# Kernel tuning notes

Measured on AMD Instinct MI355X. Metric: run time of the kernel, lower is better.

Reference implementation:

```python
import jax, jax.numpy as jnp
import numpy as np

N_NODES = 100000
N_EDGES = 1600000
HIDDEN = 128
HALF = HIDDEN // 2
LN_EPS = 1e-5


def setup_inputs() -> dict:
    key = jax.random.key(0)
    ks = jax.random.split(key, 8)
    pos = jax.random.normal(ks[0], (N_NODES, 3), dtype=jnp.float32) * 10.0
    edge_index = jax.random.randint(ks[1], (2, N_EDGES), 0, N_NODES, dtype=jnp.int64)
    batch = jnp.zeros((N_NODES,), dtype=jnp.int64)
    # spatial_encoder params: Linear(3, HALF) -> LayerNorm(HALF) -> GELU -> Linear(HALF, HALF)
    W1 = jax.random.normal(ks[2], (3, HALF), dtype=jnp.float32) * 0.3
    b1 = jax.random.normal(ks[3], (HALF,), dtype=jnp.float32) * 0.05
    ln_g = jnp.ones((HALF,), dtype=jnp.float32)
    ln_b = jnp.zeros((HALF,), dtype=jnp.float32)
    W2 = jax.random.normal(ks[4], (HALF, HALF), dtype=jnp.float32) * 0.1
    b2 = jax.random.normal(ks[5], (HALF,), dtype=jnp.float32) * 0.05
    return {"pos": pos, "edge_index": edge_index, "batch": batch,
            "W1": W1, "b1": b1, "ln_g": ln_g, "ln_b": ln_b, "W2": W2, "b2": b2}


def _layernorm(x, g, b):
    mu = jnp.mean(x, axis=-1, keepdims=True)
    var = jnp.mean((x - mu) ** 2, axis=-1, keepdims=True)
    return (x - mu) * jax.lax.rsqrt(var + LN_EPS) * g + b


def reference(pos, edge_index, batch, W1, b1, ln_g, ln_b, W2, b2):
    num_nodes = pos.shape[0]
    src, dst = edge_index[0], edge_index[1]
    rel = pos[dst] - pos[src]                              # [E, 3]
    dist = jnp.linalg.norm(rel, axis=1, keepdims=True)     # [E, 1]
    rel_n = rel / (dist + 1e-6)
    h = rel_n @ W1 + b1                                    # [E, HALF]
    h = _layernorm(h, ln_g, ln_b)
    h = jax.nn.gelu(h, approximate=False)                  # torch exact GELU
    code = h @ W2 + b2                                     # dropout is identity in eval
    agg = jax.ops.segment_sum(code, dst, num_segments=num_nodes)          # [N, HALF]
    deg = jax.ops.segment_sum(jnp.ones_like(dst, dtype=code.dtype), dst,
                              num_segments=num_nodes)
    deg = jnp.clip(deg, 1.0)
    agg = agg / deg[:, None]
    # original buffer is [N, HIDDEN]; only the first HALF channels receive updates
    out = jnp.concatenate([agg, jnp.zeros_like(agg)], axis=1)             # [N, HIDDEN]
    return out
```

## Files before the change

### kernel.cpp

```cpp
#include <hip/hip_runtime.h>
#include <math.h>

#define HALF 64
#define LN_EPS 1e-5f
#define TCAP 1024
#define PCAP 128

#define GC0 -2.3022082f
#define GC1 -0.1029438f

typedef float f32x2 __attribute__((ext_vector_type(2)));

__device__ __forceinline__ f32x2 pk_fma(f32x2 a, f32x2 b, f32x2 c) {
    f32x2 d;
    asm("v_pk_fma_f32 %0, %1, %2, %3" : "=v"(d) : "v"(a), "v"(b), "v"(c));
    return d;
}
__device__ __forceinline__ f32x2 pk_mul(f32x2 a, f32x2 b) {
    f32x2 d;
    asm("v_pk_mul_f32 %0, %1, %2" : "=v"(d) : "v"(a), "v"(b));
    return d;
}

__device__ __forceinline__ float gelu_fast(float x) {
    const float x2 = x * x;
    const float z  = x * fmaf(GC1, x2, GC0);
    const float e  = __builtin_amdgcn_exp2f(z);
    const float sg = __builtin_amdgcn_rcpf(1.0f + e);
    return x * sg;
}

__global__ void __launch_bounds__(256, 8) bin_kernel(
    const int* __restrict__ ei, int* __restrict__ tcount,
    unsigned* __restrict__ tbuf,
    const float* __restrict__ W1, const float* __restrict__ b1,
    float* __restrict__ fp, int E, int ntile)
{
    if (blockIdx.x == 0 && threadIdx.x < 64) {
        const int t = threadIdx.x;
        const float w0 = W1[t], w1 = W1[HALF + t], w2 = W1[2 * HALF + t], bb = b1[t];
        float v[14] = { w0, w1, w2, bb,
                        w0 * w0, w0 * w1, w0 * w2, w1 * w1, w1 * w2, w2 * w2,
                        w0 * bb, w1 * bb, w2 * bb, bb * bb };
#pragma unroll
        for (int j = 0; j < 14; ++j) {
            float s = v[j];
#pragma unroll
            for (int off = 32; off; off >>= 1) s += __shfl_down(s, off, 64);
            if (t == 0) fp[j] = s * (1.0f / 64.0f);
        }
    }

    const int p = blockIdx.x & 7;
    const int e4 = (blockIdx.x * 256 + threadIdx.x) * 4;
    if (e4 >= E) return;
    if (e4 + 3 < E) {
        const int4 s = *(const int4*)(ei + e4);
        const int4 d = *(const int4*)(ei + E + e4);
        const int t0 = d.x >> 4, t1 = d.y >> 4, t2 = d.z >> 4, t3 = d.w >> 4;
        const int s0 = atomicAdd(&tcount[(size_t)p * ntile + t0], 1);
        const int s1 = atomicAdd(&tcount[(size_t)p * ntile + t1], 1);
        const int s2 = atomicAdd(&tcount[(size_t)p * ntile + t2], 1);
        const int s3 = atomicAdd(&tcount[(size_t)p * ntile + t3], 1);
        if (s0 < PCAP)
            tbuf[((size_t)p * ntile + t0) * PCAP + s0] = ((unsigned)s.x << 4) | (d.x & 15);
        if (s1 < PCAP)
            tbuf[((size_t)p * ntile + t1) * PCAP + s1] = ((unsigned)s.y << 4) | (d.y & 15);
        if (s2 < PCAP)
            tbuf[((size_t)p * ntile + t2) * PCAP + s2] = ((unsigned)s.z << 4) | (d.z & 15);
        if (s3 < PCAP)
            tbuf[((size_t)p * ntile + t3) * PCAP + s3] = ((unsigned)s.w << 4) | (d.w & 15);
    } else {
        for (int e = e4; e < E; ++e) {
            const int d = ei[E + e];
            const int t = d >> 4;
            const int sl = atomicAdd(&tcount[(size_t)p * ntile + t], 1);
            if (sl < PCAP)
                tbuf[((size_t)p * ntile + t) * PCAP + sl] =
                    ((unsigned)ei[e] << 4) | (d & 15);
        }
    }
}

__global__ void __launch_bounds__(256, 6) nodeout_kernel(
    const unsigned* __restrict__ tbuf,
    const int* __restrict__ tcount,
    const float* __restrict__ pos,
    const float* __restrict__ W1, const float* __restrict__ b1,
    const float* __restrict__ ln_g, const float* __restrict__ ln_b,
    const float* __restrict__ W2, const float* __restrict__ b2,
    const float* __restrict__ fp,
    float* __restrict__ out, int N, int ntile)
{
    __shared__ __attribute__((aligned(16))) float sRx[TCAP + 64];
    __shared__ __attribute__((aligned(16))) float sRy[TCAP + 64];
    __shared__ __attribute__((aligned(16))) float sRz[TCAP + 64];
    __shared__ __attribute__((aligned(16))) float sRw[TCAP + 64];
    __shared__ __attribute__((aligned(16))) float sh[16 * 64];
    __shared__ float4 sPd[16];
    __shared__ int   lcnt[16], lofs[16], lcur[16];
    __shared__ int   pOff[9];

    const int tid = threadIdx.x;
    const int lane = tid & 63, w = tid >> 6;
    const int tile = blockIdx.x;
    const int base = tile * 16;

    if (tid < 16) {
        lcnt[tid] = 0;
        const int n = base + tid;
        if (n < N)
            sPd[tid] = make_float4(pos[3 * n], pos[3 * n + 1], pos[3 * n + 2], 0.0f);
    }
    if (tid < 8) {
        int c = tcount[(size_t)tid * ntile + tile];
        c = (c < PCAP) ? c : PCAP;
        int inc = c;
#pragma unroll
        for (int off = 1; off < 8; off <<= 1) {
            const int u = __shfl_up(inc, off, 64);
            if (tid >= off) inc += u;
        }
        pOff[tid + 1] = inc;
        if (tid == 0) pOff[0] = 0;
    }

    const float gl = ln_g[lane];
    const float C0 = gl * (W1[lane]            - fp[0]);
    const float C1 = gl * (W1[HALF + lane]     - fp[1]);
    const float C2 = gl * (W1[2 * HALF + lane] - fp[2]);
    const float C3 = gl * (b1[lane]            - fp[3]);
    const float Bl = ln_b[lane];
    const float b2l = b2[lane];
    const f32x2 C0p = { C0, C0 }, C1p = { C1, C1 };
    const f32x2 C2p = { C2, C2 }, C3p = { C3, C3 };
    const f32x2 Blp = { Bl, Bl };
    const f32x2 GC0p = { GC0, GC0 }, GC1p = { GC1, GC1 };

    const float ux = fp[0], uy = fp[1], uz = fp[2], cc = fp[3];
    const float Gxx = fp[4], Gxy = fp[5], Gxz = fp[6];
    const float Gyy = fp[7], Gyz = fp[8], Gzz = fp[9];
    const float px = fp[10], py = fp[11], pz = fp[12], q13 = fp[13];

    __syncthreads();
    const int cnt = pOff[8];

    unsigned ev0 = 0, ev1 = 0, ev2 = 0, ev3 = 0;
#define LOADE(EV, J)                                                        \
    if ((J) < cnt) {                                                        \
        int p = 0;                                                          \
        _Pragma("unroll")                                                   \
        for (int k = 1; k < 8; ++k) p += ((J) >= pOff[k]) ? 1 : 0;          \
        EV = tbuf[((size_t)p * ntile + tile) * PCAP + ((J) - pOff[p])];     \
        atomicAdd(&lcnt[EV & 15], 1);                                       \
    }
    LOADE(ev0, tid)
    LOADE(ev1, tid + 256)
    LOADE(ev2, tid + 512)
    LOADE(ev3, tid + 768)
#undef LOADE
    __syncthreads();

    if (tid < 16) {
        const int v = lcnt[tid];
        const int vp = (v + 3) & ~3;
        int inc = vp;
#pragma unroll
        for (int off = 1; off < 16; off <<= 1) {
            const int u = __shfl_up(inc, off, 64);
            if (tid >= off) inc += u;
        }
        lofs[tid] = inc - vp;
        lcur[tid] = inc - vp;
    }
    __syncthreads();

#define GEOM(EV, J)                                                         \
    if ((J) < cnt) {                                                        \
        const int s  = (int)((EV) >> 4);                                    \
        const int dl = (int)((EV) & 15);                                    \
        const float4 pd = sPd[dl];                                          \
        const float rx0 = pd.x - pos[3 * s];                                \
        const float ry0 = pd.y - pos[3 * s + 1];                            \
        const float rz0 = pd.z - pos[3 * s + 2];                            \
        const float dist = sqrtf(rx0 * rx0 + ry0 * ry0 + rz0 * rz0);        \
        const float invd = 1.0f / (dist + 1e-6f);                           \
        const float rx = rx0 * invd, ry = ry0 * invd, rz = rz0 * invd;      \
        const float mu  = fmaf(ux, rx, fmaf(uy, ry, fmaf(uz, rz, cc)));     \
        const float ev2 = Gxx * rx * rx + Gyy * ry * ry + Gzz * rz * rz     \
                        + 2.0f * (Gxy * rx * ry + Gxz * rx * rz             \
                                  + Gyz * ry * rz + px * rx + py * ry       \
                                  + pz * rz) + q13;                         \
        const float rstd = rsqrtf(ev2 - mu * mu + LN_EPS);                  \
        const int slot = atomicAdd(&lcur[dl], 1);                           \
        sRx[slot] = rx * rstd;                                              \
        sRy[slot] = ry * rstd;                                              \
        sRz[slot] = rz * rstd;                                              \
        sRw[slot] = rstd;                                                   \
    }
    GEOM(ev0, tid)
    GEOM(ev1, tid + 256)
    GEOM(ev2, tid + 512)
    GEOM(ev3, tid + 768)
#undef GEOM
    __syncthreads();

    const int n0 = base + w * 4;
    const int c0 = lcnt[w * 4 + 0], b0 = lofs[w * 4 + 0];
    const int c1 = lcnt[w * 4 + 1], b1o = lofs[w * 4 + 1];
    const int c2 = lcnt[w * 4 + 2], b2o = lofs[w * 4 + 2];
    const int c3 = lcnt[w * 4 + 3], b3o = lofs[w * 4 + 3];

#define PAIR_GELU(RXP, RYP, RZP, RWP, GA, GB)                               \
        {                                                                   \
            const f32x2 X = pk_fma(C0p, RXP, pk_fma(C1p, RYP,               \
                              pk_fma(C2p, RZP, pk_fma(C3p, RWP, Blp))));    \
            const f32x2 x2 = pk_mul(X, X);                                  \
            const f32x2 zt = pk_fma(GC1p, x2, GC0p);                        \
            const f32x2 z  = pk_mul(X, zt);                                 \
            const float e0 = __builtin_amdgcn_exp2f(z.x);                   \
            const float e1 = __builtin_amdgcn_exp2f(z.y);                   \
            const float r0 = __builtin_amdgcn_rcpf(1.0f + e0);              \
            const float r1 = __builtin_amdgcn_rcpf(1.0f + e1);              \
            GA += X.x * r0;                                                 \
            GB += X.y * r1;                                                 \
        }

#define NODE_ACC(BO, CQ, ROW)                                               \
    {                                                                       \
        const int cntn = (CQ);                                              \
        const int bo = (BO);                                                \
        float accA = 0.0f, accB = 0.0f;                                     \
        int i = 0;                                                          \
        for (; i + 4 <= cntn; i += 4) {     \
            const float4 vx = *(const float4*)(sRx + bo + i);               \
            const float4 vy = *(const float4*)(sRy + bo + i);               \
            const float4 vz = *(const float4*)(sRz + bo + i);               \
            const float4 vw = *(const float4*)(sRw + bo + i);               \
            f32x2 rxa = { vx.x, vx.y }, rxb = { vx.z, vx.w };               \
            f32x2 rya = { vy.x, vy.y }, ryb = { vy.z, vy.w };               \
            f32x2 rza = { vz.x, vz.y }, rzb = { vz.z, vz.w };               \
            f32x2 rwa = { vw.x, vw.y }, rwb = { vw.z, vw.w };               \
            PAIR_GELU(rxa, rya, rza, rwa, accA, accB)                       \
            PAIR_GELU(rxb, ryb, rzb, rwb, accA, accB)                       \
        }                                                                   \
        for (; i < cntn; ++i) {              \
            const float x = fmaf(C0, sRx[bo + i], fmaf(C1, sRy[bo + i],     \
                              fmaf(C2, sRz[bo + i],                         \
                                   fmaf(C3, sRw[bo + i], Bl))));            \
            accA += gelu_fast(x);                                           \
        }                                                                   \
        sh[(ROW) * 64 + lane] = (cntn > 0)                                  \
            ? (accA + accB) * (1.0f / (float)cntn) : 0.0f;                  \
    }

    NODE_ACC(b0,  c0, w * 4 + 0)
    NODE_ACC(b1o, c1, w * 4 + 1)
    NODE_ACC(b2o, c2, w * 4 + 2)
    NODE_ACC(b3o, c3, w * 4 + 3)
#undef NODE_ACC
#undef PAIR_GELU

    __builtin_amdgcn_sched_barrier(0);

    f32x2 wpk[32];
#pragma unroll
    for (int k = 0; k < 32; ++k) {
        wpk[k].x = W2[(2 * k)     * HALF + lane];
        wpk[k].y = W2[(2 * k + 1) * HALF + lane];
    }

#define PHASE2(Q, CQ)                                                       \
    if (n0 + (Q) < N) {                                                     \
        const float* row = sh + (w * 4 + (Q)) * 64;                         \
        f32x2 acc = { 0.0f, 0.0f };                                         \
        _Pragma("unroll")                                                   \
        for (int k4 = 0; k4 < 16; ++k4) {                                   \
            const float4 hv = *(const float4*)(row + 4 * k4);               \
            f32x2 ha = { hv.x, hv.y }, hb = { hv.z, hv.w };                 \
            acc = pk_fma(ha, wpk[2 * k4],     acc);                         \
            acc = pk_fma(hb, wpk[2 * k4 + 1], acc);                         \
        }                                                                   \
        const float res = ((CQ) > 0) ? (acc.x + acc.y) + b2l : 0.0f;        \
        float* orow = out + (size_t)(n0 + (Q)) * (2 * HALF);                \
        orow[lane] = res;                                                   \
        orow[HALF + lane] = 0.0f;                                           \
    }

    PHASE2(0, c0)
    PHASE2(1, c1)
    PHASE2(2, c2)
    PHASE2(3, c3)
#undef PHASE2
}

extern "C" void kernel_launch(void* const* d_in, const int* in_sizes, int n_in,
                              void* d_out, int out_size, void* d_ws, size_t ws_size,
                              hipStream_t stream) {
    const float* pos = (const float*)d_in[0];
    const int*   ei  = (const int*)d_in[1];
    const float* W1  = (const float*)d_in[3];
    const float* b1  = (const float*)d_in[4];
    const float* g   = (const float*)d_in[5];
    const float* b   = (const float*)d_in[6];
    const float* W2  = (const float*)d_in[7];
    const float* b2  = (const float*)d_in[8];
    float* out = (float*)d_out;

    const int N = in_sizes[0] / 3;
    const int E = in_sizes[1] / 2;
    const int ntile = (N + 15) / 16;

    unsigned* tbuf = (unsigned*)d_ws;
    int* tcount    = (int*)(tbuf + (size_t)8 * ntile * PCAP);
    float* fparams = (float*)(tcount + (size_t)8 * ntile);

    const int eb4 = (E / 4 + 255) / 256;

    hipMemsetAsync(tcount, 0, (size_t)8 * ntile * sizeof(int), stream);
    bin_kernel<<<eb4, 256, 0, stream>>>(ei, tcount, tbuf, W1, b1, fparams,
                                        E, ntile);
    nodeout_kernel<<<ntile, 256, 0, stream>>>(tbuf, tcount, pos, W1, b1, g, b,
                                              W2, b2, fparams, out, N, ntile);
}
```

Baseline: 224.6 us.

## Balance per-wave edge work and accumulate GELU outputs via LDS atomics

Replaces the per-node bucketed layout (count, prefix scan, scatter into SoA arrays, one wave per four nodes) with an unsorted AoS float4 array that tags each edge with its local destination in the low bits of rstd. Edges are split evenly across the four waves, and per-lane GELU results are accumulated into shared node rows with LDS float atomics. The mean division moves after the W2 matvec. This removes two barriers and the wave load imbalance caused by uneven node degrees, but adds many LDS atomic adds and perturbs rstd's low mantissa bits. The launch-bounds occupancy hint also drops from 6 to 4.

```diff
diff --git a/kernel.cpp b/kernel.cpp
--- a/kernel.cpp
+++ b/kernel.cpp
@@ -82,7 +82,7 @@
     }
 }
 
-__global__ void __launch_bounds__(256, 6) nodeout_kernel(
+__global__ void __launch_bounds__(256, 4) nodeout_kernel(
     const unsigned* __restrict__ tbuf,
     const int* __restrict__ tcount,
     const float* __restrict__ pos,
@@ -92,13 +92,10 @@
     const float* __restrict__ fp,
     float* __restrict__ out, int N, int ntile)
 {
-    __shared__ __attribute__((aligned(16))) float sRx[TCAP + 64];
-    __shared__ __attribute__((aligned(16))) float sRy[TCAP + 64];
-    __shared__ __attribute__((aligned(16))) float sRz[TCAP + 64];
-    __shared__ __attribute__((aligned(16))) float sRw[TCAP + 64];
-    __shared__ __attribute__((aligned(16))) float sh[16 * 64];
+    __shared__ __attribute__((aligned(16))) float4 sA[TCAP];
+    __shared__ __attribute__((aligned(16))) float  sh[16 * 64];
     __shared__ float4 sPd[16];
-    __shared__ int   lcnt[16], lofs[16], lcur[16];
+    __shared__ int   lcnt[16];
     __shared__ int   pOff[9];
 
     const int tid = threadIdx.x;
@@ -124,6 +121,7 @@
         pOff[tid + 1] = inc;
         if (tid == 0) pOff[0] = 0;
     }
+    for (int i = tid; i < 16 * 64; i += 256) sh[i] = 0.0f;
 
     const float gl = ln_g[lane];
     const float C0 = gl * (W1[lane]            - fp[0]);
@@ -145,40 +143,14 @@
     __syncthreads();
     const int cnt = pOff[8];
 
-    unsigned ev0 = 0, ev1 = 0, ev2 = 0, ev3 = 0;
-#define LOADE(EV, J)                                                        \
+#define PREP(J)                                                             \
     if ((J) < cnt) {                                                        \
         int p = 0;                                                          \
         _Pragma("unroll")                                                   \
         for (int k = 1; k < 8; ++k) p += ((J) >= pOff[k]) ? 1 : 0;          \
-        EV = tbuf[((size_t)p * ntile + tile) * PCAP + ((J) - pOff[p])];     \
-        atomicAdd(&lcnt[EV & 15], 1);                                       \
-    }
-    LOADE(ev0, tid)
-    LOADE(ev1, tid + 256)
-    LOADE(ev2, tid + 512)
-    LOADE(ev3, tid + 768)
-#undef LOADE
-    __syncthreads();
-
-    if (tid < 16) {
-        const int v = lcnt[tid];
-        const int vp = (v + 3) & ~3;
-        int inc = vp;
-#pragma unroll
-        for (int off = 1; off < 16; off <<= 1) {
-            const int u = __shfl_up(inc, off, 64);
-            if (tid >= off) inc += u;
-        }
-        lofs[tid] = inc - vp;
-        lcur[tid] = inc - vp;
-    }
-    __syncthreads();
-
-#define GEOM(EV, J)                                                         \
-    if ((J) < cnt) {                                                        \
-        const int s  = (int)((EV) >> 4);                                    \
-        const int dl = (int)((EV) & 15);                                    \
+        const unsigned v = tbuf[((size_t)p * ntile + tile) * PCAP + ((J) - pOff[p])]; \
+        const int s  = (int)(v >> 4);                                       \
+        const int dl = (int)(v & 15);                                       \
         const float4 pd = sPd[dl];                                          \
         const float rx0 = pd.x - pos[3 * s];                                \
         const float ry0 = pd.y - pos[3 * s + 1];                            \
@@ -192,74 +164,62 @@
                                   + Gyz * ry * rz + px * rx + py * ry       \
                                   + pz * rz) + q13;                         \
         const float rstd = rsqrtf(ev2 - mu * mu + LN_EPS);                  \
-        const int slot = atomicAdd(&lcur[dl], 1);                           \
-        sRx[slot] = rx * rstd;                                              \
-        sRy[slot] = ry * rstd;                                              \
-        sRz[slot] = rz * rstd;                                              \
-        sRw[slot] = rstd;                                                   \
-    }
-    GEOM(ev0, tid)
-    GEOM(ev1, tid + 256)
-    GEOM(ev2, tid + 512)
-    GEOM(ev3, tid + 768)
-#undef GEOM
+        const unsigned enc = (__float_as_uint(rstd) & ~15u) | (unsigned)dl; \
+        sA[(J)] = make_float4(rx * rstd, ry * rstd, rz * rstd,              \
+                              __uint_as_float(enc));                        \
+        atomicAdd(&lcnt[dl], 1);                                            \
+    }
+    PREP(tid)
+    PREP(tid + 256)
+    PREP(tid + 512)
+    PREP(tid + 768)
+#undef PREP
     __syncthreads();
 
-    const int n0 = base + w * 4;
-    const int c0 = lcnt[w * 4 + 0], b0 = lofs[w * 4 + 0];
-    const int c1 = lcnt[w * 4 + 1], b1o = lofs[w * 4 + 1];
-    const int c2 = lcnt[w * 4 + 2], b2o = lofs[w * 4 + 2];
-    const int c3 = lcnt[w * 4 + 3], b3o = lofs[w * 4 + 3];
-
-#define PAIR_GELU(RXP, RYP, RZP, RWP, GA, GB)                               \
+#define PAIR_GELU_OUT(RXP, RYP, RZP, RWP, G0, G1)                           \
         {                                                                   \
             const f32x2 X = pk_fma(C0p, RXP, pk_fma(C1p, RYP,               \
                               pk_fma(C2p, RZP, pk_fma(C3p, RWP, Blp))));    \
             const f32x2 x2 = pk_mul(X, X);                                  \
             const f32x2 zt = pk_fma(GC1p, x2, GC0p);                        \
             const f32x2 z  = pk_mul(X, zt);                                 \
-            const float e0 = __builtin_amdgcn_exp2f(z.x);                   \
-            const float e1 = __builtin_amdgcn_exp2f(z.y);                   \
-            const float r0 = __builtin_amdgcn_rcpf(1.0f + e0);              \
-            const float r1 = __builtin_amdgcn_rcpf(1.0f + e1);              \
-            GA += X.x * r0;                                                 \
-            GB += X.y * r1;                                                 \
-        }
-
-#define NODE_ACC(BO, CQ, ROW)                                               \
-    {                                                                       \
-        const int cntn = (CQ);                                              \
-        const int bo = (BO);                                                \
-        float accA = 0.0f, accB = 0.0f;                                     \
-        int i = 0;                                                          \
-        for (; i + 4 <= cntn; i += 4) {     \
-            const float4 vx = *(const float4*)(sRx + bo + i);               \
-            const float4 vy = *(const float4*)(sRy + bo + i);               \
-            const float4 vz = *(const float4*)(sRz + bo + i);               \
-            const float4 vw = *(const float4*)(sRw + bo + i);               \
-            f32x2 rxa = { vx.x, vx.y }, rxb = { vx.z, vx.w };               \
-            f32x2 rya = { vy.x, vy.y }, ryb = { vy.z, vy.w };               \
-            f32x2 rza = { vz.x, vz.y }, rzb = { vz.z, vz.w };               \
-            f32x2 rwa = { vw.x, vw.y }, rwb = { vw.z, vw.w };               \
-            PAIR_GELU(rxa, rya, rza, rwa, accA, accB)                       \
-            PAIR_GELU(rxb, ryb, rzb, rwb, accA, accB)                       \
-        }                                                                   \
-        for (; i < cntn; ++i) {              \
-            const float x = fmaf(C0, sRx[bo + i], fmaf(C1, sRy[bo + i],     \
-                              fmaf(C2, sRz[bo + i],                         \
-                                   fmaf(C3, sRw[bo + i], Bl))));            \
-            accA += gelu_fast(x);                                           \
-        }                                                                   \
-        sh[(ROW) * 64 + lane] = (cntn > 0)                                  \
-            ? (accA + accB) * (1.0f / (float)cntn) : 0.0f;                  \
-    }
-
-    NODE_ACC(b0,  c0, w * 4 + 0)
-    NODE_ACC(b1o, c1, w * 4 + 1)
-    NODE_ACC(b2o, c2, w * 4 + 2)
-    NODE_ACC(b3o, c3, w * 4 + 3)
-#undef NODE_ACC
-#undef PAIR_GELU
+            const float ee0 = __builtin_amdgcn_exp2f(z.x);                  \
+            const float ee1 = __builtin_amdgcn_exp2f(z.y);                  \
+            G0 = X.x * __builtin_amdgcn_rcpf(1.0f + ee0);                   \
+            G1 = X.y * __builtin_amdgcn_rcpf(1.0f + ee1);                   \
+        }
+
+    {
+        const int lo_w = ((cnt * w) >> 2) & ~1;
+        const int hi_w = (w == 3) ? cnt : ((cnt * (w + 1)) >> 2) & ~1;
+        int i = lo_w;
+        for (; i + 4 <= hi_w; i += 4) {
+            const float4 a0 = sA[i],     a1 = sA[i + 1];
+            const float4 a2 = sA[i + 2], a3 = sA[i + 3];
+            const unsigned e0 = __float_as_uint(a0.w), e1 = __float_as_uint(a1.w);
+            const unsigned e2 = __float_as_uint(a2.w), e3 = __float_as_uint(a3.w);
+            f32x2 RX0 = { a0.x, a1.x }, RY0 = { a0.y, a1.y }, RZ0 = { a0.z, a1.z };
+            f32x2 RW0 = { a0.w, a1.w };
+            f32x2 RX1 = { a2.x, a3.x }, RY1 = { a2.y, a3.y }, RZ1 = { a2.z, a3.z };
+            f32x2 RW1 = { a2.w, a3.w };
+            float g0, g1, g2, g3;
+            PAIR_GELU_OUT(RX0, RY0, RZ0, RW0, g0, g1)
+            PAIR_GELU_OUT(RX1, RY1, RZ1, RW1, g2, g3)
+            atomicAdd(&sh[(e0 & 15u) * 64 + lane], g0);
+            atomicAdd(&sh[(e1 & 15u) * 64 + lane], g1);
+            atomicAdd(&sh[(e2 & 15u) * 64 + lane], g2);
+            atomicAdd(&sh[(e3 & 15u) * 64 + lane], g3);
+        }
+        for (; i < hi_w; ++i) {
+            const float4 a = sA[i];
+            const unsigned e = __float_as_uint(a.w);
+            const float x = fmaf(C0, a.x, fmaf(C1, a.y,
+                              fmaf(C2, a.z, fmaf(C3, a.w, Bl))));
+            atomicAdd(&sh[(e & 15u) * 64 + lane], gelu_fast(x));
+        }
+    }
+#undef PAIR_GELU_OUT
+    __syncthreads();
 
     __builtin_amdgcn_sched_barrier(0);
 
@@ -270,8 +230,10 @@
         wpk[k].y = W2[(2 * k + 1) * HALF + lane];
     }
 
-#define PHASE2(Q, CQ)                                                       \
+    const int n0 = base + w * 4;
+#define PHASE2(Q)                                                           \
     if (n0 + (Q) < N) {                                                     \
+        const int cq = lcnt[w * 4 + (Q)];                                   \
         const float* row = sh + (w * 4 + (Q)) * 64;                         \
         f32x2 acc = { 0.0f, 0.0f };                                         \
         _Pragma("unroll")                                                   \
@@ -281,16 +243,17 @@
             acc = pk_fma(ha, wpk[2 * k4],     acc);                         \
             acc = pk_fma(hb, wpk[2 * k4 + 1], acc);                         \
         }                                                                   \
-        const float res = ((CQ) > 0) ? (acc.x + acc.y) + b2l : 0.0f;        \
+        const float res = (cq > 0)                                          \
+            ? (acc.x + acc.y) * (1.0f / (float)cq) + b2l : 0.0f;            \
         float* orow = out + (size_t)(n0 + (Q)) * (2 * HALF);                \
         orow[lane] = res;                                                   \
         orow[HALF + lane] = 0.0f;                                           \
     }
 
-    PHASE2(0, c0)
-    PHASE2(1, c1)
-    PHASE2(2, c2)
-    PHASE2(3, c3)
+    PHASE2(0)
+    PHASE2(1)
+    PHASE2(2)
+    PHASE2(3)
 #undef PHASE2
 }
 
```

Result: slower. 716.4 us (+218.9%).
